# Kernel optimization log

Hardware: AMD Instinct MI355X
Metric: run time of the kernel (lower is better)

The kernel has to match this reference:

```python
import jax, jax.numpy as jnp
import numpy as np

B, T, D, R, V = 8, 512, 1024, 4, 2048


def setup_inputs() -> dict:
    key = jax.random.key(0)
    k1, k2, k3, k4, k5 = jax.random.split(key, 5)
    return {
        "input_embs": jax.random.normal(k1, (B, T, D), dtype=jnp.float32),
        "label_ids": jax.random.randint(k2, (B, T), 0, V),
        "w_alpha": jax.random.normal(k3, (D, R), dtype=jnp.float32),
        "w_beta": jax.random.normal(k4, (D, R), dtype=jnp.float32),
        "w_vocab": jax.random.normal(k5, (D, V * R * R), dtype=jnp.float32),
    }


def _normalize(m, axis):
    # torch normalize_matrix: abs then divide by sum over `dim` (rows of the matrix)
    m = jnp.abs(m)
    return m / m.sum(axis=axis, keepdims=True)


def reference(input_embs, label_ids, w_alpha, w_beta, w_vocab):
    x = input_embs
    Bq, Tq, Dq = x.shape
    xf = x.reshape(-1, Dq)                                   # [B*T, D]
    alpha = (xf @ w_alpha).reshape(Bq, Tq, R).mean(1)        # [B, R]
    beta = (xf @ w_beta).reshape(Bq, Tq, R).mean(1)          # [B, R]
    core = (xf @ w_vocab).reshape(Bq, Tq, R, V, R).mean(1)   # [B, R, V, R]

    # gather core slices core[b, :, y[b,k], :] -> [B, T, R, R]
    g = jnp.take_along_axis(core.transpose(0, 2, 1, 3),      # [B, V, R, R]
                            label_ids[:, :, None, None], axis=1)
    Mn = _normalize(g, axis=2)                               # normalize over matrix rows (dim=0)

    v = _normalize(alpha, axis=1)                            # [B, R] normalized column vector
    Ms = Mn.transpose(1, 0, 2, 3)                            # [T, B, R, R]

    def step(v, M):
        return jnp.einsum('bij,bj->bi', M, v), None

    v, _ = jax.lax.scan(step, v, Ms)                         # sequential TT chain over T
    nb = _normalize(beta, axis=1)                            # [B, R]
    probs = jnp.einsum('bi,bi->b', nb, v)                    # [B]
    loss = -jnp.log(probs)
    return loss.mean()
```

## Files before the change

kernel.cpp:

```cpp
#include <hip/hip_runtime.h>
#include <math.h>

#define Bq 8
#define T 512
#define D 1024
#define R 4
#define V 2048
#define NCOL (V * R * R)
#define DSPLIT 16
#define DCHUNK (D / DSPLIT)
#define CBLK 1024

__global__ void k_xbar(const float* __restrict__ x, float* __restrict__ xbar) {
    int b   = blockIdx.x;
    int tc  = blockIdx.y;
    int tid = threadIdx.x;
    const float4* xp = (const float4*)(x + ((size_t)b * T + (size_t)tc * 16) * D) + tid;
    float4 acc = make_float4(0.f, 0.f, 0.f, 0.f);
#pragma unroll
    for (int t = 0; t < 16; ++t) {
        float4 v = xp[t * (D / 4)];
        acc.x += v.x; acc.y += v.y; acc.z += v.z; acc.w += v.w;
    }
    float* dst = xbar + b * D + tid * 4;
    atomicAdd(dst + 0, acc.x);
    atomicAdd(dst + 1, acc.y);
    atomicAdd(dst + 2, acc.z);
    atomicAdd(dst + 3, acc.w);
}

__global__ void k_core(const float* __restrict__ wv, const float* __restrict__ xbar,
                       float* __restrict__ part) {
    __shared__ float xs[Bq * DCHUNK];
    int tid  = threadIdx.x;
    int colb = blockIdx.x;
    int ds   = blockIdx.y;
    int d0   = ds * DCHUNK;

    if (tid < (Bq * DCHUNK / 4)) {
        int l  = tid * 4;
        int b  = l / DCHUNK;
        int dd = l % DCHUNK;
        *(float4*)(xs + l) = *(const float4*)(xbar + b * D + d0 + dd);
    }
    __syncthreads();

    int col = colb * CBLK + tid * 4;
    const float4* wp = (const float4*)(wv + (size_t)d0 * NCOL + col);
    float4 acc[Bq];
#pragma unroll
    for (int b = 0; b < Bq; ++b) acc[b] = make_float4(0.f, 0.f, 0.f, 0.f);

#pragma unroll 4
    for (int d = 0; d < DCHUNK; ++d) {
        float4 w = wp[(size_t)d * (NCOL / 4)];
#pragma unroll
        for (int b = 0; b < Bq; ++b) {
            float xv = xs[b * DCHUNK + d];
            acc[b].x += w.x * xv;
            acc[b].y += w.y * xv;
            acc[b].z += w.z * xv;
            acc[b].w += w.w * xv;
        }
    }

#pragma unroll
    for (int b = 0; b < Bq; ++b)
        *(float4*)(part + ((size_t)ds * Bq + b) * NCOL + col) = acc[b];
}

__global__ void k_gather(const float* __restrict__ part, const int* __restrict__ labels,
                         float* __restrict__ Mn) {
    int idx = blockIdx.x * 256 + threadIdx.x;
    int b   = idx >> 9;
    int y   = labels[idx];

    float4 g[R];
#pragma unroll
    for (int i = 0; i < R; ++i) g[i] = make_float4(0.f, 0.f, 0.f, 0.f);

    for (int ds = 0; ds < DSPLIT; ++ds) {
        const float* pb = part + ((size_t)ds * Bq + b) * NCOL + y * R;
#pragma unroll
        for (int i = 0; i < R; ++i) {
            float4 v = *(const float4*)(pb + i * (V * R));
            g[i].x += v.x; g[i].y += v.y; g[i].z += v.z; g[i].w += v.w;
        }
    }
#pragma unroll
    for (int i = 0; i < R; ++i) {
        g[i].x = fabsf(g[i].x); g[i].y = fabsf(g[i].y);
        g[i].z = fabsf(g[i].z); g[i].w = fabsf(g[i].w);
    }
    float4 cs = make_float4(g[0].x + g[1].x + g[2].x + g[3].x,
                            g[0].y + g[1].y + g[2].y + g[3].y,
                            g[0].z + g[1].z + g[2].z + g[3].z,
                            g[0].w + g[1].w + g[2].w + g[3].w);
    float4 rc = make_float4(1.f / cs.x, 1.f / cs.y, 1.f / cs.z, 1.f / cs.w);

    float* mo = Mn + (size_t)idx * 16;
#pragma unroll
    for (int i = 0; i < R; ++i) {
        float4 o = make_float4(g[i].x * rc.x, g[i].y * rc.y, g[i].z * rc.z, g[i].w * rc.w);
        *(float4*)(mo + i * 4) = o;
    }
}

__global__ void k_chain(const float* __restrict__ Mn, const float* __restrict__ xbar,
                        const float* __restrict__ wa, const float* __restrict__ wb,
                        float* __restrict__ out) {
    __shared__ float mats[Bq][32][17];
    __shared__ float abp[256];
    __shared__ float lossp[Bq];
    int tid = threadIdx.x;

    {
        int r   = tid & 3;
        int sel = (tid >> 2) & 1;
        int q   = (tid >> 3) & 3;
        int b   = tid >> 5;
        const float* w  = sel ? wb : wa;
        const float* xp = xbar + b * D;
        float s = 0.f;
#pragma unroll 8
        for (int d = q * 256; d < q * 256 + 256; ++d)
            s += xp[d] * w[d * R + r];
        abp[tid] = s;
    }

    int b = tid >> 5;
    int c = tid & 31;
    float P[R][R];
#pragma unroll
    for (int i = 0; i < R; ++i)
#pragma unroll
        for (int j = 0; j < R; ++j) P[i][j] = (i == j) ? 1.f : 0.f;

    const float* mp = Mn + ((size_t)b * T + (size_t)c * 16) * 16;
    for (int t = 0; t < 16; ++t) {
        float4 m0 = *(const float4*)(mp + t * 16 + 0);
        float4 m1 = *(const float4*)(mp + t * 16 + 4);
        float4 m2 = *(const float4*)(mp + t * 16 + 8);
        float4 m3 = *(const float4*)(mp + t * 16 + 12);
        float M[R][R] = {{m0.x, m0.y, m0.z, m0.w},
                         {m1.x, m1.y, m1.z, m1.w},
                         {m2.x, m2.y, m2.z, m2.w},
                         {m3.x, m3.y, m3.z, m3.w}};
        float N[R][R];
#pragma unroll
        for (int i = 0; i < R; ++i)
#pragma unroll
            for (int j = 0; j < R; ++j)
                N[i][j] = M[i][0] * P[0][j] + M[i][1] * P[1][j] +
                          M[i][2] * P[2][j] + M[i][3] * P[3][j];
#pragma unroll
        for (int i = 0; i < R; ++i)
#pragma unroll
            for (int j = 0; j < R; ++j) P[i][j] = N[i][j];
    }
#pragma unroll
    for (int i = 0; i < R; ++i)
#pragma unroll
        for (int j = 0; j < R; ++j) mats[b][c][i * 4 + j] = P[i][j];
    __syncthreads();

    for (int rnd = 0; rnd < 5; ++rnd) {
        int step = 1 << rnd;
        bool act = ((c & (2 * step - 1)) == 0);
        float N2[R][R];
        if (act) {
            float A[R][R], Bm[R][R];
#pragma unroll
            for (int i = 0; i < R; ++i)
#pragma unroll
                for (int j = 0; j < R; ++j) {
                    A[i][j]  = mats[b][c + step][i * 4 + j];
                    Bm[i][j] = mats[b][c][i * 4 + j];
                }
#pragma unroll
            for (int i = 0; i < R; ++i)
#pragma unroll
                for (int j = 0; j < R; ++j)
                    N2[i][j] = A[i][0] * Bm[0][j] + A[i][1] * Bm[1][j] +
                               A[i][2] * Bm[2][j] + A[i][3] * Bm[3][j];
        }
        __syncthreads();
        if (act) {
#pragma unroll
            for (int i = 0; i < R; ++i)
#pragma unroll
                for (int j = 0; j < R; ++j) mats[b][c][i * 4 + j] = N2[i][j];
        }
        __syncthreads();
    }

    if (tid < Bq) {
        int bb = tid;
        float a[R], be[R];
#pragma unroll
        for (int r = 0; r < R; ++r) {
            float sa = 0.f, sb = 0.f;
#pragma unroll
            for (int q = 0; q < 4; ++q) {
                sa += abp[(bb << 5) | (q << 3) | (0 << 2) | r];
                sb += abp[(bb << 5) | (q << 3) | (1 << 2) | r];
            }
            a[r] = sa; be[r] = sb;
        }
        float sa = fabsf(a[0]) + fabsf(a[1]) + fabsf(a[2]) + fabsf(a[3]);
        float v0[R];
#pragma unroll
        for (int r = 0; r < R; ++r) v0[r] = fabsf(a[r]) / sa;
        float v[R];
#pragma unroll
        for (int i = 0; i < R; ++i)
            v[i] = mats[bb][0][i * 4 + 0] * v0[0] + mats[bb][0][i * 4 + 1] * v0[1] +
                   mats[bb][0][i * 4 + 2] * v0[2] + mats[bb][0][i * 4 + 3] * v0[3];
        float sb = fabsf(be[0]) + fabsf(be[1]) + fabsf(be[2]) + fabsf(be[3]);
        float prob = (fabsf(be[0]) * v[0] + fabsf(be[1]) * v[1] +
                      fabsf(be[2]) * v[2] + fabsf(be[3]) * v[3]) / sb;
        lossp[bb] = -logf(prob);
    }
    __syncthreads();
    if (tid == 0) {
        float s = 0.f;
#pragma unroll
        for (int i = 0; i < Bq; ++i) s += lossp[i];
        out[0] = s * (1.f / Bq);
    }
}

extern "C" void kernel_launch(void* const* d_in, const int* in_sizes, int n_in,
                              void* d_out, int out_size, void* d_ws, size_t ws_size,
                              hipStream_t stream) {
    const float* x      = (const float*)d_in[0];
    const int*   labels = (const int*)d_in[1];
    const float* wa     = (const float*)d_in[2];
    const float* wb     = (const float*)d_in[3];
    const float* wv     = (const float*)d_in[4];
    float* out = (float*)d_out;

    float* xbar = (float*)d_ws;
    float* part = xbar + Bq * D;
    float* Mn   = part + (size_t)DSPLIT * Bq * NCOL;

    hipMemsetAsync(xbar, 0, Bq * D * sizeof(float), stream);
    k_xbar<<<dim3(Bq, 32), 256, 0, stream>>>(x, xbar);
    k_core<<<dim3(NCOL / CBLK, DSPLIT), 256, 0, stream>>>(wv, xbar, part);
    k_gather<<<Bq * T / 256, 256, 0, stream>>>(part, labels, Mn);
    k_chain<<<1, 256, 0, stream>>>(Mn, xbar, wa, wb, out);
}
```

Baseline: 267.4 us.

## Spread gather and chain work over more threads and blocks per batch

The gather kernel now assigns one matrix row per thread and computes column sums with lane shuffles, giving four times as many threads with fewer loads each. The chain kernel launches one block per batch element with 64 threads, each handling 8 steps, followed by a 6-round tree reduction. The final loss is accumulated with an atomicAdd into an output zeroed by a memset. The core GEMV unroll factor is also raised. These changes target the serial chain tail and the low parallelism of the gather stage, at the cost of an extra memset and atomics.

After: 239.8 us. 10.3% less time.

```diff
diff --git a/kernel.cpp b/kernel.cpp
--- a/kernel.cpp
+++ b/kernel.cpp
@@ -51,7 +51,7 @@
 #pragma unroll
     for (int b = 0; b < Bq; ++b) acc[b] = make_float4(0.f, 0.f, 0.f, 0.f);
 
-#pragma unroll 4
+#pragma unroll 8
     for (int d = 0; d < DCHUNK; ++d) {
         float4 w = wp[(size_t)d * (NCOL / 4)];
 #pragma unroll
@@ -71,73 +71,69 @@
 
 __global__ void k_gather(const float* __restrict__ part, const int* __restrict__ labels,
                          float* __restrict__ Mn) {
-    int idx = blockIdx.x * 256 + threadIdx.x;
-    int b   = idx >> 9;
-    int y   = labels[idx];
-
-    float4 g[R];
-#pragma unroll
-    for (int i = 0; i < R; ++i) g[i] = make_float4(0.f, 0.f, 0.f, 0.f);
-
+    int b   = blockIdx.x;
+    int tc  = blockIdx.y;
+    int tid = threadIdx.x;
+    int tl  = tid >> 2;
+    int i   = tid & 3;
+    int t   = tc * 64 + tl;
+    int y   = labels[b * T + t];
+
+    const float* pb = part + (size_t)b * NCOL + (size_t)i * (V * R) + (size_t)y * R;
+    float4 g = make_float4(0.f, 0.f, 0.f, 0.f);
+#pragma unroll
     for (int ds = 0; ds < DSPLIT; ++ds) {
-        const float* pb = part + ((size_t)ds * Bq + b) * NCOL + y * R;
-#pragma unroll
-        for (int i = 0; i < R; ++i) {
-            float4 v = *(const float4*)(pb + i * (V * R));
-            g[i].x += v.x; g[i].y += v.y; g[i].z += v.z; g[i].w += v.w;
-        }
-    }
-#pragma unroll
-    for (int i = 0; i < R; ++i) {
-        g[i].x = fabsf(g[i].x); g[i].y = fabsf(g[i].y);
-        g[i].z = fabsf(g[i].z); g[i].w = fabsf(g[i].w);
-    }
-    float4 cs = make_float4(g[0].x + g[1].x + g[2].x + g[3].x,
-                            g[0].y + g[1].y + g[2].y + g[3].y,
-                            g[0].z + g[1].z + g[2].z + g[3].z,
-                            g[0].w + g[1].w + g[2].w + g[3].w);
-    float4 rc = make_float4(1.f / cs.x, 1.f / cs.y, 1.f / cs.z, 1.f / cs.w);
-
-    float* mo = Mn + (size_t)idx * 16;
-#pragma unroll
-    for (int i = 0; i < R; ++i) {
-        float4 o = make_float4(g[i].x * rc.x, g[i].y * rc.y, g[i].z * rc.z, g[i].w * rc.w);
-        *(float4*)(mo + i * 4) = o;
-    }
+        float4 v = *(const float4*)(pb + (size_t)ds * (Bq * NCOL));
+        g.x += v.x; g.y += v.y; g.z += v.z; g.w += v.w;
+    }
+    g.x = fabsf(g.x); g.y = fabsf(g.y); g.z = fabsf(g.z); g.w = fabsf(g.w);
+
+    float sx = g.x, sy = g.y, sz = g.z, sw = g.w;
+    sx += __shfl_xor(sx, 1); sy += __shfl_xor(sy, 1);
+    sz += __shfl_xor(sz, 1); sw += __shfl_xor(sw, 1);
+    sx += __shfl_xor(sx, 2); sy += __shfl_xor(sy, 2);
+    sz += __shfl_xor(sz, 2); sw += __shfl_xor(sw, 2);
+
+    float4 o = make_float4(g.x / sx, g.y / sy, g.z / sz, g.w / sw);
+    *(float4*)(Mn + ((size_t)(b * T + t)) * 16 + i * 4) = o;
 }
 
 __global__ void k_chain(const float* __restrict__ Mn, const float* __restrict__ xbar,
                         const float* __restrict__ wa, const float* __restrict__ wb,
                         float* __restrict__ out) {
-    __shared__ float mats[Bq][32][17];
-    __shared__ float abp[256];
-    __shared__ float lossp[Bq];
+    __shared__ float mats[64][17];
+    __shared__ float abp[64];
+    int b   = blockIdx.x;
     int tid = threadIdx.x;
 
     {
         int r   = tid & 3;
         int sel = (tid >> 2) & 1;
-        int q   = (tid >> 3) & 3;
-        int b   = tid >> 5;
+        int seg = tid >> 3;
         const float* w  = sel ? wb : wa;
         const float* xp = xbar + b * D;
         float s = 0.f;
 #pragma unroll 8
-        for (int d = q * 256; d < q * 256 + 256; ++d)
+        for (int d = seg * 128; d < seg * 128 + 128; ++d)
             s += xp[d] * w[d * R + r];
         abp[tid] = s;
     }
 
-    int b = tid >> 5;
-    int c = tid & 31;
+    int c = tid;
+    const float* mp = Mn + ((size_t)b * T + (size_t)c * 8) * 16;
     float P[R][R];
-#pragma unroll
-    for (int i = 0; i < R; ++i)
-#pragma unroll
-        for (int j = 0; j < R; ++j) P[i][j] = (i == j) ? 1.f : 0.f;
-
-    const float* mp = Mn + ((size_t)b * T + (size_t)c * 16) * 16;
-    for (int t = 0; t < 16; ++t) {
+    {
+        float4 m0 = *(const float4*)(mp + 0);
+        float4 m1 = *(const float4*)(mp + 4);
+        float4 m2 = *(const float4*)(mp + 8);
+        float4 m3 = *(const float4*)(mp + 12);
+        P[0][0]=m0.x; P[0][1]=m0.y; P[0][2]=m0.z; P[0][3]=m0.w;
+        P[1][0]=m1.x; P[1][1]=m1.y; P[1][2]=m1.z; P[1][3]=m1.w;
+        P[2][0]=m2.x; P[2][1]=m2.y; P[2][2]=m2.z; P[2][3]=m2.w;
+        P[3][0]=m3.x; P[3][1]=m3.y; P[3][2]=m3.z; P[3][3]=m3.w;
+    }
+#pragma unroll
+    for (int t = 1; t < 8; ++t) {
         float4 m0 = *(const float4*)(mp + t * 16 + 0);
         float4 m1 = *(const float4*)(mp + t * 16 + 4);
         float4 m2 = *(const float4*)(mp + t * 16 + 8);
@@ -161,10 +157,10 @@
 #pragma unroll
     for (int i = 0; i < R; ++i)
 #pragma unroll
-        for (int j = 0; j < R; ++j) mats[b][c][i * 4 + j] = P[i][j];
+        for (int j = 0; j < R; ++j) mats[c][i * 4 + j] = P[i][j];
     __syncthreads();
 
-    for (int rnd = 0; rnd < 5; ++rnd) {
+    for (int rnd = 0; rnd < 6; ++rnd) {
         int step = 1 << rnd;
         bool act = ((c & (2 * step - 1)) == 0);
         float N2[R][R];
@@ -174,8 +170,8 @@
             for (int i = 0; i < R; ++i)
 #pragma unroll
                 for (int j = 0; j < R; ++j) {
-                    A[i][j]  = mats[b][c + step][i * 4 + j];
-                    Bm[i][j] = mats[b][c][i * 4 + j];
+                    A[i][j]  = mats[c + step][i * 4 + j];
+                    Bm[i][j] = mats[c][i * 4 + j];
                 }
 #pragma unroll
             for (int i = 0; i < R; ++i)
@@ -189,21 +185,20 @@
 #pragma unroll
             for (int i = 0; i < R; ++i)
 #pragma unroll
-                for (int j = 0; j < R; ++j) mats[b][c][i * 4 + j] = N2[i][j];
+                for (int j = 0; j < R; ++j) mats[c][i * 4 + j] = N2[i][j];
         }
         __syncthreads();
     }
 
-    if (tid < Bq) {
-        int bb = tid;
+    if (tid == 0) {
         float a[R], be[R];
 #pragma unroll
         for (int r = 0; r < R; ++r) {
             float sa = 0.f, sb = 0.f;
 #pragma unroll
-            for (int q = 0; q < 4; ++q) {
-                sa += abp[(bb << 5) | (q << 3) | (0 << 2) | r];
-                sb += abp[(bb << 5) | (q << 3) | (1 << 2) | r];
+            for (int seg = 0; seg < 8; ++seg) {
+                sa += abp[(seg << 3) | r];
+                sb += abp[(seg << 3) | 4 | r];
             }
             a[r] = sa; be[r] = sb;
         }
@@ -214,19 +209,12 @@
         float v[R];
 #pragma unroll
         for (int i = 0; i < R; ++i)
-            v[i] = mats[bb][0][i * 4 + 0] * v0[0] + mats[bb][0][i * 4 + 1] * v0[1] +
-                   mats[bb][0][i * 4 + 2] * v0[2] + mats[bb][0][i * 4 + 3] * v0[3];
+            v[i] = mats[0][i * 4 + 0] * v0[0] + mats[0][i * 4 + 1] * v0[1] +
+                   mats[0][i * 4 + 2] * v0[2] + mats[0][i * 4 + 3] * v0[3];
         float sb = fabsf(be[0]) + fabsf(be[1]) + fabsf(be[2]) + fabsf(be[3]);
         float prob = (fabsf(be[0]) * v[0] + fabsf(be[1]) * v[1] +
                       fabsf(be[2]) * v[2] + fabsf(be[3]) * v[3]) / sb;
-        lossp[bb] = -logf(prob);
-    }
-    __syncthreads();
-    if (tid == 0) {
-        float s = 0.f;
-#pragma unroll
-        for (int i = 0; i < Bq; ++i) s += lossp[i];
-        out[0] = s * (1.f / Bq);
+        atomicAdd(out, -logf(prob) * 0.125f);
     }
 }
 
@@ -245,8 +233,9 @@
     float* Mn   = part + (size_t)DSPLIT * Bq * NCOL;
 
     hipMemsetAsync(xbar, 0, Bq * D * sizeof(float), stream);
+    hipMemsetAsync(out, 0, sizeof(float), stream);
     k_xbar<<<dim3(Bq, 32), 256, 0, stream>>>(x, xbar);
     k_core<<<dim3(NCOL / CBLK, DSPLIT), 256, 0, stream>>>(wv, xbar, part);
-    k_gather<<<Bq * T / 256, 256, 0, stream>>>(part, labels, Mn);
-    k_chain<<<1, 256, 0, stream>>>(Mn, xbar, wa, wb, out);
-}
+    k_gather<<<dim3(Bq, T / 64), 256, 0, stream>>>(part, labels, Mn);
+    k_chain<<<Bq, 64, 0, stream>>>(Mn, xbar, wa, wb, out);
+}
```
